# Kernel tuning notes

Measured on AMD Instinct MI355X. Metric: run time of the kernel, lower is better.

## Reference

```python
import jax, jax.numpy as jnp
import numpy as np

EMBED_DIM = 384
ROUTER_HIDDEN = 64
NUM_EXPERTS = 4
TOP_K = 1
TEMPERATURE = 2.0  # buffer value, clamp(min=0.1) is a no-op here
LN_EPS = 1e-5


def setup_inputs() -> dict:
    key = jax.random.key(0)
    kx, k1, k2 = jax.random.split(key, 3)
    x = jax.random.normal(kx, (16, 8192, EMBED_DIM), dtype=jnp.float32)
    ln_w = jnp.ones((EMBED_DIM,), dtype=jnp.float32)
    ln_b = jnp.zeros((EMBED_DIM,), dtype=jnp.float32)
    # kaiming-uniform-ish init, scale irrelevant for correctness testing
    w1 = jax.random.normal(k1, (EMBED_DIM, ROUTER_HIDDEN), dtype=jnp.float32) / np.sqrt(EMBED_DIM)
    w2 = jax.random.normal(k2, (ROUTER_HIDDEN, NUM_EXPERTS), dtype=jnp.float32) / np.sqrt(ROUTER_HIDDEN)
    return {"x": x, "ln_w": ln_w, "ln_b": ln_b, "w1": w1, "w2": w2}


def reference(x, ln_w, ln_b, w1, w2):
    T = jnp.maximum(jnp.float32(TEMPERATURE), 0.1)
    # LayerNorm over last dim
    mu = jnp.mean(x, axis=-1, keepdims=True)
    var = jnp.mean(jnp.square(x - mu), axis=-1, keepdims=True)
    h = (x - mu) * jax.lax.rsqrt(var + LN_EPS) * ln_w + ln_b
    # MLP gate: Linear(384->64, no bias) -> GELU(exact) -> Linear(64->4, no bias)
    h = jax.nn.gelu(jnp.einsum("bld,dh->blh", h, w1), approximate=False)
    logits = jnp.einsum("blh,he->ble", h, w2) / T
    probs = jax.nn.softmax(logits, axis=-1)  # (B, L, E)
    _, indices = jax.lax.top_k(probs, TOP_K)  # (B, L, top_k)
    B, L = indices.shape[0], indices.shape[1]
    # load-balance aux loss (f is non-differentiable, as under torch.no_grad)
    one_hot = jax.nn.one_hot(indices, NUM_EXPERTS, dtype=jnp.float32)  # (B, L, K, E)
    f = jnp.sum(one_hot, axis=(0, 1, 2)) / (B * L * TOP_K)  # (E,)
    P = jnp.mean(probs, axis=(0, 1))  # (E,)
    aux_loss = NUM_EXPERTS * jnp.sum(f * P)
    return probs, indices, aux_loss, probs
```

## Files before the change

### kernel.cpp

```cpp
#include <hip/hip_runtime.h>
#include <math.h>

#define EMBED 384
#define HID 64
#define NE 4
#define TPB 512
#define MT 8
#define JS 8
#define JPT 8
#define TOKB 512

#define WLN_F   (EMBED * HID)
#define W2_OFF  (WLN_F)
#define C1_OFF  (W2_OFF + HID * NE)
#define C2_OFF  (C1_OFF + HID)
#define PART_OFF (C2_OFF + HID)
#define RED_OFF (PART_OFF + 2 * TPB)
#define SMEM_FLOATS (RED_OFF + 2 * NE)

__global__ void
__attribute__((amdgpu_flat_work_group_size(TPB, TPB), amdgpu_waves_per_eu(1, 2)))
router_main(
    const float* __restrict__ x, const float* __restrict__ lnw,
    const float* __restrict__ lnb, const float* __restrict__ w1,
    const float* __restrict__ w2, float* __restrict__ out,
    float* __restrict__ ws, int ntok)
{
  extern __shared__ float smem[];
  float* wln = smem;
  float* w2s = smem + W2_OFF;
  float* c1s = smem + C1_OFF;
  float* c2s = smem + C2_OFF;
  float* part = smem + PART_OFF;
  float* red = smem + RED_OFF;

  const int tid = (int)threadIdx.x;

  {
    const float4* src = reinterpret_cast<const float4*>(w1);
    float4* dst = reinterpret_cast<float4*>(wln);
    #pragma unroll
    for (int k = 0; k < (WLN_F / 4) / TPB; ++k) {
      const int f4 = tid + k * TPB;
      const float sc = lnw[f4 >> 4];
      float4 v = src[f4];
      v.x *= sc; v.y *= sc; v.z *= sc; v.w *= sc;
      dst[f4] = v;
    }
  }
  if (tid < HID * NE / 4) {
    reinterpret_cast<float4*>(w2s)[tid] = reinterpret_cast<const float4*>(w2)[tid];
  }
  if (tid < 2 * NE) red[tid] = 0.f;
  __syncthreads();

  {
    const int j = tid & 63;
    const int dpart = tid >> 6;
    float c1p = 0.f, c2p = 0.f;
    #pragma unroll 8
    for (int k = 0; k < EMBED / 8; ++k) {
      const int d = dpart * (EMBED / 8) + k;
      c1p += wln[d * HID + j];
      c2p = fmaf(lnb[d], w1[d * HID + j], c2p);
    }
    part[dpart * 64 + j] = c1p;
    part[TPB + dpart * 64 + j] = c2p;
  }
  __syncthreads();
  if (tid < HID) {
    float a = 0.f, b = 0.f;
    #pragma unroll
    for (int p = 0; p < 8; ++p) {
      a += part[p * 64 + tid];
      b += part[TPB + p * 64 + tid];
    }
    c1s[tid] = a;
    c2s[tid] = b;
  }
  __syncthreads();

  const int lane = tid & 63;
  const int wv = tid >> 6;
  const int tg = lane >> 3;
  const int jg = lane & 7;
  const int wbase = (int)blockIdx.x * TOKB + wv * 64;
  const int t0 = wbase + tg * MT;
  const int joff = jg * JPT;

  const float* __restrict__ xrow = x + (size_t)t0 * EMBED;

  float acc[MT][JPT];
  #pragma unroll
  for (int m = 0; m < MT; ++m)
    #pragma unroll
    for (int j = 0; j < JPT; ++j) acc[m][j] = 0.f;
  float s[MT], s2[MT];
  #pragma unroll
  for (int m = 0; m < MT; ++m) { s[m] = 0.f; s2[m] = 0.f; }

  #pragma unroll 2
  for (int dq = 0; dq < EMBED / 4; ++dq) {
    const int d = dq * 4;
    float4 xv[MT];
    #pragma unroll
    for (int m = 0; m < MT; ++m)
      xv[m] = *reinterpret_cast<const float4*>(xrow + (size_t)m * EMBED + d);
    #pragma unroll
    for (int m = 0; m < MT; ++m) {
      s[m] += (xv[m].x + xv[m].y) + (xv[m].z + xv[m].w);
      s2[m] = fmaf(xv[m].x, xv[m].x, s2[m]);
      s2[m] = fmaf(xv[m].y, xv[m].y, s2[m]);
      s2[m] = fmaf(xv[m].z, xv[m].z, s2[m]);
      s2[m] = fmaf(xv[m].w, xv[m].w, s2[m]);
    }
    #pragma unroll
    for (int dd = 0; dd < 4; ++dd) {
      const float* wr = wln + (d + dd) * HID + joff;
      float4 wa = *reinterpret_cast<const float4*>(wr);
      float4 wb = *reinterpret_cast<const float4*>(wr + 4);
      #pragma unroll
      for (int m = 0; m < MT; ++m) {
        const float xx = (dd == 0) ? xv[m].x : (dd == 1) ? xv[m].y
                       : (dd == 2) ? xv[m].z : xv[m].w;
        acc[m][0] = fmaf(xx, wa.x, acc[m][0]);
        acc[m][1] = fmaf(xx, wa.y, acc[m][1]);
        acc[m][2] = fmaf(xx, wa.z, acc[m][2]);
        acc[m][3] = fmaf(xx, wa.w, acc[m][3]);
        acc[m][4] = fmaf(xx, wb.x, acc[m][4]);
        acc[m][5] = fmaf(xx, wb.y, acc[m][5]);
        acc[m][6] = fmaf(xx, wb.z, acc[m][6]);
        acc[m][7] = fmaf(xx, wb.w, acc[m][7]);
      }
    }
  }

  float mu[MT], rstd[MT];
  #pragma unroll
  for (int m = 0; m < MT; ++m) {
    mu[m] = s[m] * (1.f / EMBED);
    const float var = fmaf(-mu[m], mu[m], s2[m] * (1.f / EMBED));
    rstd[m] = rsqrtf(var + 1e-5f);
  }

  float logit[MT][NE];
  #pragma unroll
  for (int m = 0; m < MT; ++m)
    #pragma unroll
    for (int e = 0; e < NE; ++e) logit[m][e] = 0.f;

  #pragma unroll
  for (int jj = 0; jj < JPT; ++jj) {
    const int j = joff + jj;
    const float c1 = c1s[j];
    const float c2 = c2s[j];
    float4 wv = *reinterpret_cast<const float4*>(w2s + j * NE);
    #pragma unroll
    for (int m = 0; m < MT; ++m) {
      const float hid = fmaf(rstd[m], fmaf(-mu[m], c1, acc[m][jj]), c2);
      const float g = 0.5f * hid * (1.f + erff(hid * 0.7071067811865475f));
      logit[m][0] = fmaf(g, wv.x, logit[m][0]);
      logit[m][1] = fmaf(g, wv.y, logit[m][1]);
      logit[m][2] = fmaf(g, wv.z, logit[m][2]);
      logit[m][3] = fmaf(g, wv.w, logit[m][3]);
    }
  }

  #pragma unroll
  for (int m = 0; m < MT; ++m)
    #pragma unroll
    for (int e = 0; e < NE; ++e) {
      logit[m][e] += __shfl_xor(logit[m][e], 1);
      logit[m][e] += __shfl_xor(logit[m][e], 2);
      logit[m][e] += __shfl_xor(logit[m][e], 4);
    }

  float l[NE];
  #pragma unroll
  for (int e = 0; e < NE; ++e) {
    float v = logit[0][e];
    v = (jg == 1) ? logit[1][e] : v;
    v = (jg == 2) ? logit[2][e] : v;
    v = (jg == 3) ? logit[3][e] : v;
    v = (jg == 4) ? logit[4][e] : v;
    v = (jg == 5) ? logit[5][e] : v;
    v = (jg == 6) ? logit[6][e] : v;
    v = (jg == 7) ? logit[7][e] : v;
    l[e] = v * 0.5f;
  }
  const int mytok = wbase + lane;

  const float mx = fmaxf(fmaxf(l[0], l[1]), fmaxf(l[2], l[3]));
  const float e0 = expf(l[0] - mx), e1 = expf(l[1] - mx),
              e2 = expf(l[2] - mx), e3 = expf(l[3] - mx);
  const float inv = 1.f / (e0 + e1 + e2 + e3);
  const float p0 = e0 * inv, p1 = e1 * inv, p2 = e2 * inv, p3 = e3 * inv;

  int best = 0; float bp = p0;
  if (p1 > bp) { bp = p1; best = 1; }
  if (p2 > bp) { bp = p2; best = 2; }
  if (p3 > bp) { bp = p3; best = 3; }

  if (mytok < ntok) {
    *reinterpret_cast<float4*>(out + (size_t)mytok * 4) = make_float4(p0, p1, p2, p3);
    out[(size_t)ntok * 4 + mytok] = (float)best;
    float* o3 = out + (size_t)ntok * 5 + 1 + (size_t)mytok * 4;
    o3[0] = p0; o3[1] = p1; o3[2] = p2; o3[3] = p3;
  }

  float psum[NE] = {p0, p1, p2, p3};
  float pcnt[NE];
  pcnt[0] = (best == 0) ? 1.f : 0.f;
  pcnt[1] = (best == 1) ? 1.f : 0.f;
  pcnt[2] = (best == 2) ? 1.f : 0.f;
  pcnt[3] = (best == 3) ? 1.f : 0.f;

  #pragma unroll
  for (int e = 0; e < NE; ++e) {
    float a = psum[e], c = pcnt[e];
    #pragma unroll
    for (int off = 32; off; off >>= 1) {
      a += __shfl_xor(a, off);
      c += __shfl_xor(c, off);
    }
    if (lane == 0) {
      atomicAdd(&red[e], a);
      atomicAdd(&red[NE + e], c);
    }
  }
  __syncthreads();
  if (tid < 2 * NE) atomicAdd(&ws[tid], red[tid]);
}

__global__ void router_finalize(const float* __restrict__ ws,
                                float* __restrict__ out, int ntok)
{
  if (threadIdx.x == 0 && blockIdx.x == 0) {
    const float invN = 1.f / (float)ntok;
    float aux = 0.f;
    #pragma unroll
    for (int e = 0; e < NE; ++e)
      aux = fmaf(ws[NE + e] * invN, ws[e] * invN, aux);
    out[(size_t)ntok * 5] = (float)NE * aux;
  }
}

extern "C" void kernel_launch(void* const* d_in, const int* in_sizes, int n_in,
                              void* d_out, int out_size, void* d_ws, size_t ws_size,
                              hipStream_t stream) {
  const float* x   = (const float*)d_in[0];
  const float* lnw = (const float*)d_in[1];
  const float* lnb = (const float*)d_in[2];
  const float* w1  = (const float*)d_in[3];
  const float* w2  = (const float*)d_in[4];
  float* out = (float*)d_out;
  float* ws  = (float*)d_ws;

  const int ntok = in_sizes[0] / EMBED;

  hipMemsetAsync(d_ws, 0, 2 * NE * sizeof(float), stream);

  const int blocks = (ntok + TOKB - 1) / TOKB;
  const size_t smem_bytes = SMEM_FLOATS * sizeof(float);
  router_main<<<blocks, TPB, smem_bytes, stream>>>(x, lnw, lnb, w1, w2, out, ws, ntok);
  router_finalize<<<1, 64, 0, stream>>>(ws, out, ntok);
}
```

Baseline: 138.3 us.

## Split hidden dim across 16 lanes, double block threads, dedupe LN stats

Doubles the block to 1024 threads and halves the per-thread hidden slice to 4 columns with 16 lanes per token group, so each wave covers 32 tokens instead of 64. This cuts the accumulator register count and targets higher occupancy for hiding memory latency. LayerNorm sums are now computed once per token by an owner lane and broadcast with shuffles, instead of redundantly by every lane. The cost is an extra shuffle-reduction step, twice the shared-memory weight reads per FMA, and half the lanes sitting idle in the epilogue.

Measured after the change: 180.4 us. 1.3x slower.

```diff
diff --git a/kernel.cpp b/kernel.cpp
--- a/kernel.cpp
+++ b/kernel.cpp
@@ -4,10 +4,10 @@
 #define EMBED 384
 #define HID 64
 #define NE 4
-#define TPB 512
+#define TPB 1024
 #define MT 8
-#define JS 8
-#define JPT 8
+#define JS 16
+#define JPT 4
 #define TOKB 512
 
 #define WLN_F   (EMBED * HID)
@@ -19,7 +19,7 @@
 #define SMEM_FLOATS (RED_OFF + 2 * NE)
 
 __global__ void
-__attribute__((amdgpu_flat_work_group_size(TPB, TPB), amdgpu_waves_per_eu(1, 2)))
+__attribute__((amdgpu_flat_work_group_size(TPB, TPB), amdgpu_waves_per_eu(4, 4)))
 router_main(
     const float* __restrict__ x, const float* __restrict__ lnw,
     const float* __restrict__ lnb, const float* __restrict__ w1,
@@ -59,8 +59,8 @@
     const int dpart = tid >> 6;
     float c1p = 0.f, c2p = 0.f;
     #pragma unroll 8
-    for (int k = 0; k < EMBED / 8; ++k) {
-      const int d = dpart * (EMBED / 8) + k;
+    for (int k = 0; k < EMBED / 16; ++k) {
+      const int d = dpart * (EMBED / 16) + k;
       c1p += wln[d * HID + j];
       c2p = fmaf(lnb[d], w1[d * HID + j], c2p);
     }
@@ -71,7 +71,7 @@
   if (tid < HID) {
     float a = 0.f, b = 0.f;
     #pragma unroll
-    for (int p = 0; p < 8; ++p) {
+    for (int p = 0; p < 16; ++p) {
       a += part[p * 64 + tid];
       b += part[TPB + p * 64 + tid];
     }
@@ -82,65 +82,64 @@
 
   const int lane = tid & 63;
   const int wv = tid >> 6;
-  const int tg = lane >> 3;
-  const int jg = lane & 7;
-  const int wbase = (int)blockIdx.x * TOKB + wv * 64;
+  const int tg = lane >> 4;
+  const int jg = lane & 15;
+  const int wbase = (int)blockIdx.x * TOKB + wv * 32;
   const int t0 = wbase + tg * MT;
   const int joff = jg * JPT;
 
   const float* __restrict__ xrow = x + (size_t)t0 * EMBED;
+  const float* __restrict__ xown = x + (size_t)(t0 + (jg & 7)) * EMBED;
 
   float acc[MT][JPT];
   #pragma unroll
   for (int m = 0; m < MT; ++m)
     #pragma unroll
     for (int j = 0; j < JPT; ++j) acc[m][j] = 0.f;
-  float s[MT], s2[MT];
-  #pragma unroll
-  for (int m = 0; m < MT; ++m) { s[m] = 0.f; s2[m] = 0.f; }
-
-  #pragma unroll 2
+  float s = 0.f, s2 = 0.f;
+
   for (int dq = 0; dq < EMBED / 4; ++dq) {
     const int d = dq * 4;
+
+    {
+      float4 xo = *reinterpret_cast<const float4*>(xown + d);
+      s += (xo.x + xo.y) + (xo.z + xo.w);
+      s2 = fmaf(xo.x, xo.x, s2);
+      s2 = fmaf(xo.y, xo.y, s2);
+      s2 = fmaf(xo.z, xo.z, s2);
+      s2 = fmaf(xo.w, xo.w, s2);
+    }
+
     float4 xv[MT];
     #pragma unroll
     for (int m = 0; m < MT; ++m)
       xv[m] = *reinterpret_cast<const float4*>(xrow + (size_t)m * EMBED + d);
-    #pragma unroll
-    for (int m = 0; m < MT; ++m) {
-      s[m] += (xv[m].x + xv[m].y) + (xv[m].z + xv[m].w);
-      s2[m] = fmaf(xv[m].x, xv[m].x, s2[m]);
-      s2[m] = fmaf(xv[m].y, xv[m].y, s2[m]);
-      s2[m] = fmaf(xv[m].z, xv[m].z, s2[m]);
-      s2[m] = fmaf(xv[m].w, xv[m].w, s2[m]);
-    }
+
     #pragma unroll
     for (int dd = 0; dd < 4; ++dd) {
-      const float* wr = wln + (d + dd) * HID + joff;
-      float4 wa = *reinterpret_cast<const float4*>(wr);
-      float4 wb = *reinterpret_cast<const float4*>(wr + 4);
+      const float4 wv4 = *reinterpret_cast<const float4*>(wln + (d + dd) * HID + joff);
       #pragma unroll
       for (int m = 0; m < MT; ++m) {
         const float xx = (dd == 0) ? xv[m].x : (dd == 1) ? xv[m].y
                        : (dd == 2) ? xv[m].z : xv[m].w;
-        acc[m][0] = fmaf(xx, wa.x, acc[m][0]);
-        acc[m][1] = fmaf(xx, wa.y, acc[m][1]);
-        acc[m][2] = fmaf(xx, wa.z, acc[m][2]);
-        acc[m][3] = fmaf(xx, wa.w, acc[m][3]);
-        acc[m][4] = fmaf(xx, wb.x, acc[m][4]);
-        acc[m][5] = fmaf(xx, wb.y, acc[m][5]);
-        acc[m][6] = fmaf(xx, wb.z, acc[m][6]);
-        acc[m][7] = fmaf(xx, wb.w, acc[m][7]);
+        acc[m][0] = fmaf(xx, wv4.x, acc[m][0]);
+        acc[m][1] = fmaf(xx, wv4.y, acc[m][1]);
+        acc[m][2] = fmaf(xx, wv4.z, acc[m][2]);
+        acc[m][3] = fmaf(xx, wv4.w, acc[m][3]);
       }
     }
   }
 
+  const float mu_own = s * (1.f / EMBED);
+  const float var_own = fmaf(-mu_own, mu_own, s2 * (1.f / EMBED));
+  const float rstd_own = rsqrtf(var_own + 1e-5f);
+
+  const int gb = lane & ~15;
   float mu[MT], rstd[MT];
   #pragma unroll
   for (int m = 0; m < MT; ++m) {
-    mu[m] = s[m] * (1.f / EMBED);
-    const float var = fmaf(-mu[m], mu[m], s2[m] * (1.f / EMBED));
-    rstd[m] = rsqrtf(var + 1e-5f);
+    mu[m]   = __shfl(mu_own,   gb + m);
+    rstd[m] = __shfl(rstd_own, gb + m);
   }
 
   float logit[MT][NE];
@@ -173,22 +172,25 @@
       logit[m][e] += __shfl_xor(logit[m][e], 1);
       logit[m][e] += __shfl_xor(logit[m][e], 2);
       logit[m][e] += __shfl_xor(logit[m][e], 4);
-    }
-
+      logit[m][e] += __shfl_xor(logit[m][e], 8);
+    }
+
+  const int mown = jg & 7;
   float l[NE];
   #pragma unroll
   for (int e = 0; e < NE; ++e) {
     float v = logit[0][e];
-    v = (jg == 1) ? logit[1][e] : v;
-    v = (jg == 2) ? logit[2][e] : v;
-    v = (jg == 3) ? logit[3][e] : v;
-    v = (jg == 4) ? logit[4][e] : v;
-    v = (jg == 5) ? logit[5][e] : v;
-    v = (jg == 6) ? logit[6][e] : v;
-    v = (jg == 7) ? logit[7][e] : v;
+    v = (mown == 1) ? logit[1][e] : v;
+    v = (mown == 2) ? logit[2][e] : v;
+    v = (mown == 3) ? logit[3][e] : v;
+    v = (mown == 4) ? logit[4][e] : v;
+    v = (mown == 5) ? logit[5][e] : v;
+    v = (mown == 6) ? logit[6][e] : v;
+    v = (mown == 7) ? logit[7][e] : v;
     l[e] = v * 0.5f;
   }
-  const int mytok = wbase + lane;
+  const int mytok = t0 + mown;
+  const bool owner = (jg < 8);
 
   const float mx = fmaxf(fmaxf(l[0], l[1]), fmaxf(l[2], l[3]));
   const float e0 = expf(l[0] - mx), e1 = expf(l[1] - mx),
@@ -201,19 +203,20 @@
   if (p2 > bp) { bp = p2; best = 2; }
   if (p3 > bp) { bp = p3; best = 3; }
 
-  if (mytok < ntok) {
+  if (owner && mytok < ntok) {
     *reinterpret_cast<float4*>(out + (size_t)mytok * 4) = make_float4(p0, p1, p2, p3);
     out[(size_t)ntok * 4 + mytok] = (float)best;
     float* o3 = out + (size_t)ntok * 5 + 1 + (size_t)mytok * 4;
     o3[0] = p0; o3[1] = p1; o3[2] = p2; o3[3] = p3;
   }
 
-  float psum[NE] = {p0, p1, p2, p3};
+  const float wsc = owner ? 1.f : 0.f;
+  float psum[NE] = {p0 * wsc, p1 * wsc, p2 * wsc, p3 * wsc};
   float pcnt[NE];
-  pcnt[0] = (best == 0) ? 1.f : 0.f;
-  pcnt[1] = (best == 1) ? 1.f : 0.f;
-  pcnt[2] = (best == 2) ? 1.f : 0.f;
-  pcnt[3] = (best == 3) ? 1.f : 0.f;
+  pcnt[0] = (owner && best == 0) ? 1.f : 0.f;
+  pcnt[1] = (owner && best == 1) ? 1.f : 0.f;
+  pcnt[2] = (owner && best == 2) ? 1.f : 0.f;
+  pcnt[3] = (owner && best == 3) ? 1.f : 0.f;
 
   #pragma unroll
   for (int e = 0; e < NE; ++e) {
```
